# Performance work log

Measured on AMD Instinct MI355X. Metric: run time of the kernel, lower is better.

## Reference

```python
import jax, jax.numpy as jnp
import numpy as np

RADIUS = 1.3
COARSE = 64
FINE = 2
N_ATOMS = 64
SH_DIM = 9
DATA_DIM = SH_DIM * 3 + 1  # 28
N_INTRS = COARSE * 3 * 2 * FINE  # 768
STEP = (RADIUS * 2.0 / COARSE / FINE) / 2.0
BATCH = 1024


def sh_basis(d):
    # real spherical harmonics basis, degree 2 (9 coeffs), on normalized dirs
    d = d / jnp.linalg.norm(d, axis=-1, keepdims=True)
    x, y, z = d[..., 0], d[..., 1], d[..., 2]
    C0 = 0.28209479177387814
    C1 = 0.4886025119029199
    C20, C21, C22, C23, C24 = (1.0925484305920792, -1.0925484305920792,
                               0.31539156525252005, -1.0925484305920792,
                               0.5462742152960396)
    return jnp.stack([
        C0 * jnp.ones_like(x), -C1 * y, C1 * z, -C1 * x,
        C20 * x * y, C21 * y * z, C22 * (2.0 * z * z - x * x - y * y),
        C23 * x * z, C24 * (x * x - y * y)
    ], axis=-1)


def dict_interp(grid, atoms, pts):
    # l2_interp_v2: coarse-voxel dictionary coeffs x trilinear fine-atom interp
    # pts: [P,3] in [0,1)
    P = pts.shape[0]
    pc = pts * COARSE
    c = jnp.clip(jnp.floor(pc), 0, COARSE - 1).astype(jnp.int32)
    local = pc - c.astype(pts.dtype)  # position inside coarse voxel, [0,1)
    clin = (c[:, 0] * COARSE + c[:, 1]) * COARSE + c[:, 2]
    coeff = grid[clin]                              # [P, A]
    # project dictionary coeffs through atoms for every fine cell: [P, FINE^3, D]
    proj = jnp.einsum('pa,fad->pfd', coeff, atoms)
    u = local * FINE - 0.5
    f = jnp.floor(u)
    t = u - f
    i0 = jnp.clip(f, 0, FINE - 1).astype(jnp.int32)
    i1 = jnp.clip(f + 1.0, 0, FINE - 1).astype(jnp.int32)
    idx = jnp.stack([i0, i1], axis=-1)              # [P,3,2]
    w = jnp.stack([1.0 - t, t], axis=-1)            # [P,3,2]
    rows = jnp.arange(P)
    out = jnp.zeros((P, DATA_DIM), dtype=pts.dtype)
    for kx in (0, 1):
        for ky in (0, 1):
            for kz in (0, 1):
                lin = (idx[:, 0, kx] * FINE + idx[:, 1, ky]) * FINE + idx[:, 2, kz]
                wgt = w[:, 0, kx] * w[:, 1, ky] * w[:, 2, kz]
                out = out + wgt[:, None] * proj[rows, lin]
    return out


def _forward(rays_o, rays_d, grid, atoms):
    dt = rays_o.dtype
    # ---- sample_proposal (no grad) ----
    off_pos = (RADIUS - rays_o) / rays_d
    off_neg = (-RADIUS - rays_o) / rays_d
    start = jnp.max(jnp.minimum(off_pos, off_neg), axis=-1, keepdims=True)
    intersections = jax.lax.stop_gradient(
        start + jnp.arange(N_INTRS, dtype=dt)[None, :] * STEP)  # [B, 768]
    tr = intersections[:, :-1]  # [B, 767]
    pts = rays_o[:, None, :] + tr[..., None] * rays_d[:, None, :]  # [B,n,3]
    mask = jnp.all((pts > -RADIUS) & (pts < RADIUS), axis=-1)      # [B,n]
    pts = jax.lax.stop_gradient(pts)
    B, n = tr.shape
    # normalized coords in [0,1); masked-out points are clipped then zeroed later
    p = jnp.clip((pts + RADIUS) / (2.0 * RADIUS), 0.0, 1.0 - 1e-6).reshape(-1, 3)
    data = dict_interp(grid, atoms, p).reshape(B, n, DATA_DIM)
    # masked_scatter of sigma <=> dense compute + where(mask, ., 0)
    sigma = jnp.where(mask, jax.nn.relu(data[..., -1]), 0.0)
    dists = (intersections[:, 1:] - intersections[:, :-1]) * \
        jnp.linalg.norm(rays_d, axis=-1, keepdims=True)
    alpha = 1.0 - jnp.exp(-sigma * dists)
    trans = jnp.cumprod(1.0 - alpha + 1e-10, axis=-1)
    trans = jnp.concatenate([jnp.ones_like(trans[:, :1]), trans[:, :-1]], axis=-1)
    abs_light = alpha * trans  # per-sample weights
    sh_mult = sh_basis(rays_d)                      # [B, 9]
    sh = data[..., :-1].reshape(B, n, 3, SH_DIM)
    rgb_samp = jnp.einsum('bnck,bk->bnc', sh, sh_mult)
    rgb_samp = jax.nn.sigmoid(jnp.where(mask[..., None], rgb_samp, 0.0))
    comp = jnp.sum(abs_light[..., None] * rgb_samp, axis=1)  # [B,3]
    acc = jnp.sum(abs_light, axis=1)
    rgb = comp + (1.0 - acc)[:, None]  # white background
    depth = jnp.sum(abs_light * tr, axis=1)
    return rgb, alpha, depth


def setup_inputs():
    key = jax.random.key(0)
    k0, k1, k2, k3 = jax.random.split(key, 4)
    o = jax.random.normal(k0, (BATCH, 3), dtype=jnp.float32)
    o = o / jnp.linalg.norm(o, axis=-1, keepdims=True) * 2.5
    d = -o + 0.3 * jax.random.normal(k1, (BATCH, 3), dtype=jnp.float32)
    d = d / jnp.linalg.norm(d, axis=-1, keepdims=True)
    grid = 0.01 * jax.random.normal(k2, (COARSE ** 3, N_ATOMS), dtype=jnp.float32)
    atoms_sh = jax.random.uniform(k3, (FINE ** 3, N_ATOMS, DATA_DIM - 1), dtype=jnp.float32)
    atoms = jnp.concatenate(
        [atoms_sh, jnp.full((FINE ** 3, N_ATOMS, 1), 0.01, dtype=jnp.float32)], axis=-1)
    return {"rays_o": o, "rays_d": d, "grid": grid, "atoms": atoms, "grid_id": 0}


def reference(rays_o, rays_d, grid, atoms, grid_id):
    # grid_id selects among num_scenes grids; num_scenes=1 so grid is pre-selected
    return _forward(rays_o, rays_d, grid, atoms)
```

## Files before the change

kernel.cpp:

```cpp
#include <hip/hip_runtime.h>
#include <hip/hip_bf16.h>

#define RADIUS_F 1.3f
#define NSAMP 767
#define STEPF 0.01015625f
#define BATCH 1024

typedef __attribute__((ext_vector_type(8))) short short8;
typedef __attribute__((ext_vector_type(4))) float floatx4;

static __device__ __forceinline__ unsigned pkbf(float a, float b) {
    union { __hip_bfloat162 h; unsigned u; } cvt;
    cvt.h = __float22bfloat162_rn(make_float2(a, b));
    return cvt.u;
}

static __device__ __forceinline__ float coset4_sum(float p) {
    int q4 = __builtin_amdgcn_update_dpp(0, __float_as_int(p), 0x124, 0xf, 0xf, true);
    p = p + __int_as_float(q4);
    int q8 = __builtin_amdgcn_update_dpp(0, __float_as_int(p), 0x128, 0xf, 0xf, true);
    return p + __int_as_float(q8);
}

__launch_bounds__(512, 8)
__global__ void plenoxels_fwd(const float* __restrict__ rays_o,
                              const float* __restrict__ rays_d,
                              const float* __restrict__ grid,
                              const float* __restrict__ atoms,
                              float* __restrict__ out)
{
    __shared__ __align__(16) __hip_bfloat16 BpL[32 * 64];
    __shared__ float Wf[768 * 9];
    __shared__ __align__(16) __hip_bfloat16 alphaL[768];
    __shared__ __align__(16) __hip_bfloat16 rgbL[768 * 3];

    const int tid  = threadIdx.x;
    const int ray  = blockIdx.x;
    const int lane = tid & 63;
    const int w    = tid >> 6;
    const int m    = lane & 15;
    const int quad = lane >> 4;

    const float ox = rays_o[ray * 3 + 0], oy = rays_o[ray * 3 + 1], oz = rays_o[ray * 3 + 2];
    const float dx = rays_d[ray * 3 + 0], dy = rays_d[ray * 3 + 1], dz = rays_d[ray * 3 + 2];

    float start;
    {
        float a0 = (RADIUS_F - ox) / dx, b0 = (-RADIUS_F - ox) / dx;
        float a1 = (RADIUS_F - oy) / dy, b1 = (-RADIUS_F - oy) / dy;
        float a2 = (RADIUS_F - oz) / dz, b2 = (-RADIUS_F - oz) / dz;
        start = fmaxf(fminf(a0, b0), fmaxf(fminf(a1, b1), fminf(a2, b2)));
    }
    const float dnorm = sqrtf(dx * dx + dy * dy + dz * dz);
    const float dist = STEPF * dnorm;

    auto geom = [&](int s) -> int {
        float tr = start + (float)s * STEPF;
        float px = ox + tr * dx, py = oy + tr * dy, pz = oz + tr * dz;
        int mask = (px > -RADIUS_F) & (px < RADIUS_F) &
                   (py > -RADIUS_F) & (py < RADIUS_F) &
                   (pz > -RADIUS_F) & (pz < RADIUS_F) & (s < NSAMP);
        float maskf = mask ? 1.f : 0.f;
        const float sc = 1.0f / (2.0f * RADIUS_F);
        float qx = fminf(fmaxf((px + RADIUS_F) * sc, 0.f), 1.0f - 1e-6f);
        float qy = fminf(fmaxf((py + RADIUS_F) * sc, 0.f), 1.0f - 1e-6f);
        float qz = fminf(fmaxf((pz + RADIUS_F) * sc, 0.f), 1.0f - 1e-6f);
        float pcx = qx * 64.f, pcy = qy * 64.f, pcz = qz * 64.f;
        float cx = fminf(floorf(pcx), 63.f);
        float cy = fminf(floorf(pcy), 63.f);
        float cz = fminf(floorf(pcz), 63.f);
        float lx = pcx - cx, ly = pcy - cy, lz = pcz - cz;
        int clin = (((int)cx * 64) + (int)cy) * 64 + (int)cz;
        float xw0, xw1, yw0, yw1, zw0, zw1;
        {
            float u = lx * 2.f - 0.5f, fF = floorf(u), t = u - fF;
            xw0 = (fF < 0.f) ? 1.f : ((fF > 0.f) ? 0.f : 1.f - t);
            xw1 = (fF < 0.f) ? 0.f : ((fF > 0.f) ? 1.f : t);
        }
        {
            float u = ly * 2.f - 0.5f, fF = floorf(u), t = u - fF;
            yw0 = (fF < 0.f) ? 1.f : ((fF > 0.f) ? 0.f : 1.f - t);
            yw1 = (fF < 0.f) ? 0.f : ((fF > 0.f) ? 1.f : t);
        }
        {
            float u = lz * 2.f - 0.5f, fF = floorf(u), t = u - fF;
            zw0 = (fF < 0.f) ? 1.f : ((fF > 0.f) ? 0.f : 1.f - t);
            zw1 = (fF < 0.f) ? 0.f : ((fF > 0.f) ? 1.f : t);
        }
        xw0 *= maskf; xw1 *= maskf;
        float* wr = &Wf[s * 9];
        wr[0] = xw0 * yw0 * zw0;
        wr[1] = xw0 * yw0 * zw1;
        wr[2] = xw0 * yw1 * zw0;
        wr[3] = xw0 * yw1 * zw1;
        wr[4] = xw1 * yw0 * zw0;
        wr[5] = xw1 * yw0 * zw1;
        wr[6] = xw1 * yw1 * zw0;
        wr[7] = xw1 * yw1 * zw1;
        return clin;
    };

    int clinA = geom(w * 96 + lane);
    int clinB = 0;
    if (lane < 32) clinB = geom(w * 96 + 64 + lane);

    const float4* g4 = (const float4*)grid;
    float4 cv0, cv1, cv2, cv3;
    {
        int clinC = __shfl(clinA, m, 64);
        const float4* gp = g4 + (clinC << 4) + (quad << 2);
        cv0 = gp[0]; cv1 = gp[1]; cv2 = gp[2]; cv3 = gp[3];
    }

    {
        float shm[9];
        float inv = 1.0f / dnorm;
        float nx = dx * inv, ny = dy * inv, nz = dz * inv;
        shm[0] = 0.28209479177387814f;
        shm[1] = -0.4886025119029199f * ny;
        shm[2] = 0.4886025119029199f * nz;
        shm[3] = -0.4886025119029199f * nx;
        shm[4] = 1.0925484305920792f * nx * ny;
        shm[5] = -1.0925484305920792f * ny * nz;
        shm[6] = 0.31539156525252005f * (2.f * nz * nz - nx * nx - ny * ny);
        shm[7] = -1.0925484305920792f * nx * nz;
        shm[8] = 0.5462742152960396f * (nx * nx - ny * ny);
        for (int idx = tid; idx < 2048; idx += 512) {
            int col = idx >> 6, a = idx & 63;
            int f = col >> 2, c = col & 3;
            const float* base = atoms + (f * 64 + a) * 28;
            float sv;
            if (c == 3) sv = base[27];
            else {
                sv = 0.f;
                #pragma unroll
                for (int i = 0; i < 9; ++i) sv = fmaf(base[c * 9 + i], shm[i], sv);
            }
            BpL[col * 64 + a] = __float2bfloat16(sv);
        }
    }
    __syncthreads();

    short8 bq00, bq01, bq10, bq11;
    {
        const short* bs = (const short*)BpL;
        const short* p0 = bs + m * 64 + (quad << 4);
        bq00 = *(const short8*)(p0);
        bq01 = *(const short8*)(p0 + 8);
        const short* p1 = bs + (16 + m) * 64 + (quad << 4);
        bq10 = *(const short8*)(p1);
        bq11 = *(const short8*)(p1 + 8);
    }

    float* out_rgb   = out;
    float* out_alpha = out + BATCH * 3;
    float* out_depth = out + BATCH * 3 + BATCH * NSAMP;
    const int f0 = m >> 2;

    #pragma unroll
    for (int t = 0; t < 6; ++t) {
        union { unsigned u[4]; short8 s; } a0, a1;
        a0.u[0] = pkbf(cv0.x, cv0.y); a0.u[1] = pkbf(cv0.z, cv0.w);
        a0.u[2] = pkbf(cv1.x, cv1.y); a0.u[3] = pkbf(cv1.z, cv1.w);
        a1.u[0] = pkbf(cv2.x, cv2.y); a1.u[1] = pkbf(cv2.z, cv2.w);
        a1.u[2] = pkbf(cv3.x, cv3.y); a1.u[3] = pkbf(cv3.z, cv3.w);

        if (t < 5) {
            int tn = t + 1;
            int clinC = (tn < 4) ? __shfl(clinA, (tn << 4) + m, 64)
                                 : __shfl(clinB, ((tn - 4) << 4) + m, 64);
            const float4* gp = g4 + (clinC << 4) + (quad << 2);
            cv0 = gp[0]; cv1 = gp[1]; cv2 = gp[2]; cv3 = gp[3];
        }

        floatx4 acc0 = {0.f, 0.f, 0.f, 0.f};
        floatx4 acc1 = {0.f, 0.f, 0.f, 0.f};
        acc0 = __builtin_amdgcn_mfma_f32_16x16x32_bf16(a0.s, bq00, acc0, 0, 0, 0);
        acc0 = __builtin_amdgcn_mfma_f32_16x16x32_bf16(a1.s, bq01, acc0, 0, 0, 0);
        acc1 = __builtin_amdgcn_mfma_f32_16x16x32_bf16(a0.s, bq10, acc1, 0, 0, 0);
        acc1 = __builtin_amdgcn_mfma_f32_16x16x32_bf16(a1.s, bq11, acc1, 0, 0, 0);

        #pragma unroll
        for (int r = 0; r < 4; ++r) {
            int s = w * 96 + (t << 4) + (quad << 2) + r;
            const float* wr = &Wf[s * 9];
            float p = wr[f0] * acc0[r] + wr[4 + f0] * acc1[r];
            p = coset4_sum(p);
            if (s < NSAMP) {
                if (m == 3) {
                    float al = 1.f - __expf(-fmaxf(p, 0.f) * dist);
                    out_alpha[ray * NSAMP + s] = al;
                    alphaL[s] = __float2bfloat16(al);
                } else if (m < 3) {
                    rgbL[s * 3 + m] = __float2bfloat16(1.f / (1.f + __expf(-p)));
                }
            }
        }
    }

    __syncthreads();

    if (tid < 64) {
        int sA = tid * 12;
        int sB = min(sA + 12, NSAMP);
        float prod = 1.f;
        for (int s = sA; s < sB; ++s)
            prod *= (1.f - __bfloat162float(alphaL[s]) + 1e-10f);

        float incl = prod;
        #pragma unroll
        for (int off = 1; off < 64; off <<= 1) {
            float v = __shfl_up(incl, off, 64);
            if (tid >= off) incl *= v;
        }
        float excl = __shfl_up(incl, 1, 64);
        if (tid == 0) excl = 1.f;

        float trans = excl;
        float c0 = 0.f, c1 = 0.f, c2 = 0.f, acc = 0.f, dep = 0.f;
        for (int s = sA; s < sB; ++s) {
            float a = __bfloat162float(alphaL[s]);
            float wgt = a * trans;
            c0 += wgt * __bfloat162float(rgbL[s * 3 + 0]);
            c1 += wgt * __bfloat162float(rgbL[s * 3 + 1]);
            c2 += wgt * __bfloat162float(rgbL[s * 3 + 2]);
            acc += wgt;
            dep += wgt * (start + (float)s * STEPF);
            trans *= (1.f - a + 1e-10f);
        }
        #pragma unroll
        for (int off = 1; off < 64; off <<= 1) {
            c0  += __shfl_xor(c0, off, 64);
            c1  += __shfl_xor(c1, off, 64);
            c2  += __shfl_xor(c2, off, 64);
            acc += __shfl_xor(acc, off, 64);
            dep += __shfl_xor(dep, off, 64);
        }
        if (tid == 0) {
            float bg = 1.f - acc;
            out_rgb[ray * 3 + 0] = c0 + bg;
            out_rgb[ray * 3 + 1] = c1 + bg;
            out_rgb[ray * 3 + 2] = c2 + bg;
            out_depth[ray] = dep;
        }
    }
}

extern "C" void kernel_launch(void* const* d_in, const int* in_sizes, int n_in,
                              void* d_out, int out_size, void* d_ws, size_t ws_size,
                              hipStream_t stream) {
    const float* rays_o = (const float*)d_in[0];
    const float* rays_d = (const float*)d_in[1];
    const float* grid   = (const float*)d_in[2];
    const float* atoms  = (const float*)d_in[3];
    float* out = (float*)d_out;
    hipLaunchKernelGGL(plenoxels_fwd, dim3(BATCH), dim3(512), 0, stream,
                       rays_o, rays_d, grid, atoms, out);
}
```

Measured before the change: 120.7 us.

## Parallelize compositing scan across six waves and pack fine weights as fp16 pairs

The final transmittance scan and compositing, which one wave previously ran serially over 12 samples per lane, is spread over 384 threads at two samples each. It uses a per-wave scan plus a cross-wave prefix through shared memory and a shared-memory reduction of the partial sums. The per-sample trilinear weights are stored as packed fp16 pairs in 5 words per sample instead of 9 floats, which cuts LDS footprint and turns the MFMA epilogue's two weight loads into one. This adds two block barriers and reduces the precision of the interpolation weights.

```diff
diff --git a/kernel.cpp b/kernel.cpp
--- a/kernel.cpp
+++ b/kernel.cpp
@@ -8,11 +8,24 @@
 
 typedef __attribute__((ext_vector_type(8))) short short8;
 typedef __attribute__((ext_vector_type(4))) float floatx4;
+typedef __fp16 fp16x2 __attribute__((ext_vector_type(2)));
 
 static __device__ __forceinline__ unsigned pkbf(float a, float b) {
     union { __hip_bfloat162 h; unsigned u; } cvt;
     cvt.h = __float22bfloat162_rn(make_float2(a, b));
     return cvt.u;
+}
+static __device__ __forceinline__ unsigned pkh(float a, float b) {
+    union { fp16x2 h; unsigned u; } c;
+    c.h = __builtin_amdgcn_cvt_pkrtz(a, b);
+    return c.u;
+}
+static __device__ __forceinline__ float2 uph(unsigned u) {
+    union { unsigned u; fp16x2 h; } c; c.u = u;
+    return make_float2((float)c.h.x, (float)c.h.y);
+}
+static __device__ __forceinline__ float bfhi(unsigned u) {
+    union { unsigned u; float f; } c; c.u = u << 16; return c.f;
 }
 
 static __device__ __forceinline__ float coset4_sum(float p) {
@@ -30,9 +43,11 @@
                               float* __restrict__ out)
 {
     __shared__ __align__(16) __hip_bfloat16 BpL[32 * 64];
-    __shared__ float Wf[768 * 9];
-    __shared__ __align__(16) __hip_bfloat16 alphaL[768];
-    __shared__ __align__(16) __hip_bfloat16 rgbL[768 * 3];
+    __shared__ unsigned WpU[768 * 5];
+    __shared__ __align__(4) __hip_bfloat16 alphaL[768];
+    __shared__ __align__(4) __hip_bfloat16 rgbL[768 * 3];
+    __shared__ float wprodL[8];
+    __shared__ float partL[8][5];
 
     const int tid  = threadIdx.x;
     const int ray  = blockIdx.x;
@@ -88,15 +103,12 @@
             zw1 = (fF < 0.f) ? 0.f : ((fF > 0.f) ? 1.f : t);
         }
         xw0 *= maskf; xw1 *= maskf;
-        float* wr = &Wf[s * 9];
-        wr[0] = xw0 * yw0 * zw0;
-        wr[1] = xw0 * yw0 * zw1;
-        wr[2] = xw0 * yw1 * zw0;
-        wr[3] = xw0 * yw1 * zw1;
-        wr[4] = xw1 * yw0 * zw0;
-        wr[5] = xw1 * yw0 * zw1;
-        wr[6] = xw1 * yw1 * zw0;
-        wr[7] = xw1 * yw1 * zw1;
+        float g0 = yw0 * zw0, g1 = yw0 * zw1, g2 = yw1 * zw0, g3 = yw1 * zw1;
+        unsigned* wr = &WpU[s * 5];
+        wr[0] = pkh(xw0 * g0, xw1 * g0);
+        wr[1] = pkh(xw0 * g1, xw1 * g1);
+        wr[2] = pkh(xw0 * g2, xw1 * g2);
+        wr[3] = pkh(xw0 * g3, xw1 * g3);
         return clin;
     };
 
@@ -183,65 +195,93 @@
         #pragma unroll
         for (int r = 0; r < 4; ++r) {
             int s = w * 96 + (t << 4) + (quad << 2) + r;
-            const float* wr = &Wf[s * 9];
-            float p = wr[f0] * acc0[r] + wr[4 + f0] * acc1[r];
+            float2 wab = uph(WpU[s * 5 + f0]);
+            float p = wab.x * acc0[r] + wab.y * acc1[r];
             p = coset4_sum(p);
-            if (s < NSAMP) {
-                if (m == 3) {
-                    float al = 1.f - __expf(-fmaxf(p, 0.f) * dist);
-                    out_alpha[ray * NSAMP + s] = al;
-                    alphaL[s] = __float2bfloat16(al);
-                } else if (m < 3) {
-                    rgbL[s * 3 + m] = __float2bfloat16(1.f / (1.f + __expf(-p)));
-                }
+            if (m == 3) {
+                float al = 1.f - __expf(-fmaxf(p, 0.f) * dist);
+                if (s < NSAMP) out_alpha[ray * NSAMP + s] = al;
+                alphaL[s] = __float2bfloat16(al);
+            } else if (m < 3) {
+                rgbL[s * 3 + m] = __float2bfloat16(1.f / (1.f + __expf(-p)));
             }
         }
     }
 
     __syncthreads();
 
-    if (tid < 64) {
-        int sA = tid * 12;
-        int sB = min(sA + 12, NSAMP);
-        float prod = 1.f;
-        for (int s = sA; s < sB; ++s)
-            prod *= (1.f - __bfloat162float(alphaL[s]) + 1e-10f);
-
-        float incl = prod;
+    {
+        const bool act = (tid < 384);
+        const int s0 = tid * 2;
+        float a0 = 0.f, a1 = 0.f;
+        if (act) {
+            unsigned aa = *(const unsigned*)&alphaL[s0];
+            a0 = bfhi(aa & 0xffff);
+            a1 = bfhi(aa >> 16);
+        }
+        float pr = (1.f - a0 + 1e-10f) * (1.f - a1 + 1e-10f);
+
+        float incl = pr;
         #pragma unroll
         for (int off = 1; off < 64; off <<= 1) {
             float v = __shfl_up(incl, off, 64);
-            if (tid >= off) incl *= v;
-        }
+            if (lane >= off) incl *= v;
+        }
+        if (lane == 63) wprodL[w] = incl;
+        __syncthreads();
+
+        float base = 1.f;
+        #pragma unroll
+        for (int ww = 0; ww < 5; ++ww)
+            if (w > ww) base *= wprodL[ww];
         float excl = __shfl_up(incl, 1, 64);
-        if (tid == 0) excl = 1.f;
-
-        float trans = excl;
-        float c0 = 0.f, c1 = 0.f, c2 = 0.f, acc = 0.f, dep = 0.f;
-        for (int s = sA; s < sB; ++s) {
-            float a = __bfloat162float(alphaL[s]);
-            float wgt = a * trans;
-            c0 += wgt * __bfloat162float(rgbL[s * 3 + 0]);
-            c1 += wgt * __bfloat162float(rgbL[s * 3 + 1]);
-            c2 += wgt * __bfloat162float(rgbL[s * 3 + 2]);
-            acc += wgt;
-            dep += wgt * (start + (float)s * STEPF);
-            trans *= (1.f - a + 1e-10f);
+        if (lane == 0) excl = 1.f;
+        float trans = base * excl;
+
+        float c0 = 0.f, c1 = 0.f, c2 = 0.f, accw = 0.f, dep = 0.f;
+        if (act) {
+            unsigned u01 = *(const unsigned*)&rgbL[s0 * 3];
+            unsigned u23 = *(const unsigned*)&rgbL[s0 * 3 + 2];
+            unsigned u45 = *(const unsigned*)&rgbL[s0 * 3 + 4];
+            float w0 = a0 * trans;
+            c0 += w0 * bfhi(u01 & 0xffff);
+            c1 += w0 * bfhi(u01 >> 16);
+            c2 += w0 * bfhi(u23 & 0xffff);
+            accw += w0;
+            dep += w0 * (start + (float)s0 * STEPF);
+            trans *= (1.f - a0 + 1e-10f);
+            float w1 = a1 * trans;
+            c0 += w1 * bfhi(u23 >> 16);
+            c1 += w1 * bfhi(u45 & 0xffff);
+            c2 += w1 * bfhi(u45 >> 16);
+            accw += w1;
+            dep += w1 * (start + (float)(s0 + 1) * STEPF);
         }
         #pragma unroll
         for (int off = 1; off < 64; off <<= 1) {
-            c0  += __shfl_xor(c0, off, 64);
-            c1  += __shfl_xor(c1, off, 64);
-            c2  += __shfl_xor(c2, off, 64);
-            acc += __shfl_xor(acc, off, 64);
-            dep += __shfl_xor(dep, off, 64);
-        }
+            c0   += __shfl_xor(c0, off, 64);
+            c1   += __shfl_xor(c1, off, 64);
+            c2   += __shfl_xor(c2, off, 64);
+            accw += __shfl_xor(accw, off, 64);
+            dep  += __shfl_xor(dep, off, 64);
+        }
+        if (lane == 0) {
+            partL[w][0] = c0; partL[w][1] = c1; partL[w][2] = c2;
+            partL[w][3] = accw; partL[w][4] = dep;
+        }
+        __syncthreads();
         if (tid == 0) {
-            float bg = 1.f - acc;
-            out_rgb[ray * 3 + 0] = c0 + bg;
-            out_rgb[ray * 3 + 1] = c1 + bg;
-            out_rgb[ray * 3 + 2] = c2 + bg;
-            out_depth[ray] = dep;
+            float C0 = 0.f, C1 = 0.f, C2 = 0.f, AC = 0.f, DP = 0.f;
+            #pragma unroll
+            for (int ww = 0; ww < 6; ++ww) {
+                C0 += partL[ww][0]; C1 += partL[ww][1]; C2 += partL[ww][2];
+                AC += partL[ww][3]; DP += partL[ww][4];
+            }
+            float bg = 1.f - AC;
+            out_rgb[ray * 3 + 0] = C0 + bg;
+            out_rgb[ray * 3 + 1] = C1 + bg;
+            out_rgb[ray * 3 + 2] = C2 + bg;
+            out_depth[ray] = DP;
         }
     }
 }
```

After: 121.9 us. About the same (+1.0%).
